# Optimization experiments

Hardware: AMD Instinct MI355X
Metric: run time of the kernel (lower is better)

Reference implementation:

```python
import jax, jax.numpy as jnp
import numpy as np
import math

N_HEAD = 4
NORM_GROUPS = 16
EPS = 1e-5


def setup_inputs() -> dict:
    key = jax.random.key(0)
    ks = jax.random.split(key, 4)
    B, C, H, W = 2, 256, 64, 64
    return {
        "input": jax.random.normal(ks[0], (B, C, H, W), dtype=jnp.float32),
        "gn_weight": jnp.ones((C,), dtype=jnp.float32),
        "gn_bias": jnp.zeros((C,), dtype=jnp.float32),
        # 1x1 convs are plain channel matmuls: weight [out_ch, in_ch]
        "qkv_weight": jax.random.normal(ks[1], (3 * C, C), dtype=jnp.float32) / math.sqrt(C),
        "out_weight": jax.random.normal(ks[2], (C, C), dtype=jnp.float32) / math.sqrt(C),
        "out_bias": jnp.zeros((C,), dtype=jnp.float32),
    }


def _group_norm(x, weight, bias):
    B, C, H, W = x.shape
    g = x.reshape(B, NORM_GROUPS, C // NORM_GROUPS, H, W)
    mu = g.mean(axis=(2, 3, 4), keepdims=True)
    var = g.var(axis=(2, 3, 4), keepdims=True)
    g = (g - mu) * jax.lax.rsqrt(var + EPS)
    return g.reshape(B, C, H, W) * weight[:, None, None] + bias[:, None, None]


def reference(input, gn_weight, gn_bias, qkv_weight, out_weight, out_bias):
    B, C, H, W = input.shape
    head_dim = C // N_HEAD
    x = _group_norm(input, gn_weight, gn_bias)
    # 1x1 conv (no bias) -> [B, 3C, H, W] -> [B, n_head, 3*head_dim, H, W]
    qkv = jnp.einsum('bchw,oc->bohw', x, qkv_weight)
    qkv = qkv.reshape(B, N_HEAD, 3 * head_dim, H, W)
    q, k, v = jnp.split(qkv, 3, axis=2)
    # full spatial attention; note: scale is sqrt(channel), as in the source
    attn = jnp.einsum('bnchw,bncyx->bnhwyx', q, k) / math.sqrt(C)
    attn = jax.nn.softmax(attn.reshape(B, N_HEAD, H, W, H * W), axis=-1)
    attn = attn.reshape(B, N_HEAD, H, W, H, W)
    out = jnp.einsum('bnhwyx,bncyx->bnchw', attn, v).reshape(B, C, H, W)
    out = jnp.einsum('bchw,oc->bohw', out, out_weight) + out_bias[:, None, None]
    return out + input
```

## Files before the change

### kernel.cpp

```cpp
#include <hip/hip_runtime.h>

typedef __bf16        bf16x8 __attribute__((ext_vector_type(8)));
typedef float         f32x4  __attribute__((ext_vector_type(4)));
typedef unsigned short u16x4 __attribute__((ext_vector_type(4)));
typedef unsigned short u16x8 __attribute__((ext_vector_type(8)));
typedef unsigned int  u32x4  __attribute__((ext_vector_type(4)));

#define MFMA16(a,b,c) __builtin_amdgcn_mfma_f32_16x16x32_bf16((a),(b),(c),0,0,0)

static __device__ __forceinline__ unsigned short f2bf(float f) {
  unsigned int u = __builtin_bit_cast(unsigned int, f);
  u += 0x7fffu + ((u >> 16) & 1u);
  return (unsigned short)(u >> 16);
}
static __device__ __forceinline__ unsigned int pk2rne(float a, float b) {
  return (unsigned int)f2bf(a) | ((unsigned int)f2bf(b) << 16);
}
static __device__ __forceinline__ unsigned int pkrn(float a, float b) {
#if __has_builtin(__builtin_amdgcn_cvt_pk_bf16_f32)
  auto r = __builtin_amdgcn_cvt_pk_bf16_f32(a, b);
  return __builtin_bit_cast(unsigned int, r);
#else
  return pk2rne(a, b);
#endif
}
static __device__ __forceinline__ bf16x8 as_bf(u32x4 v) {
  return __builtin_bit_cast(bf16x8, v);
}
static __device__ __forceinline__ float bf2f(unsigned short u) {
  return __builtin_bit_cast(float, ((unsigned int)u) << 16);
}

#define SDIM 4096
#define CDIM 256
#define NHEAD 4
#define HDIM 64
#define NBATCH 2
#define KSPLIT 4

__global__ __launch_bounds__(256) void k_prep(const float* __restrict__ x,
                                              const float* __restrict__ wq,
                                              const float* __restrict__ wo,
                                              unsigned short* __restrict__ wqf,
                                              unsigned short* __restrict__ wof,
                                              float2* __restrict__ Sp) {
  int j = blockIdx.x, i = threadIdx.x;
  if (j < 256) {
    const float* p = x + (size_t)(j >> 3) * 65536 + (size_t)(j & 7) * 8192;
    float s = 0.f, sq = 0.f;
#pragma unroll
    for (int r = 0; r < 8; ++r) {
      float4 v = *(const float4*)(p + (r * 256 + i) * 4);
      s  += v.x + v.y + v.z + v.w;
      sq += v.x * v.x + v.y * v.y + v.z * v.z + v.w * v.w;
    }
    __shared__ float rs[256], rq[256];
    rs[i] = s; rq[i] = sq;
    __syncthreads();
    for (int off = 128; off > 0; off >>= 1) {
      if (i < off) { rs[i] += rs[i + off]; rq[i] += rq[i + off]; }
      __syncthreads();
    }
    if (i == 0) Sp[j] = make_float2(rs[0], rq[0]);
  } else {
    int t = (j - 256) * 256 + i;
#pragma unroll
    for (int u = 0; u < 2; ++u) {
      int G = t * 2 + u;
      const float* src; unsigned short* dst;
      if (G < 24576) {
        int tile = G >> 6, l = G & 63;
        src = wq + (size_t)((tile >> 3) * 16 + (l & 15)) * 256 + (tile & 7) * 32 + (l >> 4) * 8;
        dst = wqf + (size_t)G * 8;
      } else {
        int G2 = G - 24576, tile = G2 >> 6, l = G2 & 63;
        src = wo + (size_t)((tile >> 3) * 16 + (l & 15)) * 256 + (tile & 7) * 32 + (l >> 4) * 8;
        dst = wof + (size_t)G2 * 8;
      }
      float4 v0 = *(const float4*)src, v1 = *(const float4*)(src + 4);
      u16x8 r;
      r[0] = f2bf(v0.x); r[1] = f2bf(v0.y); r[2] = f2bf(v0.z); r[3] = f2bf(v0.w);
      r[4] = f2bf(v1.x); r[5] = f2bf(v1.y); r[6] = f2bf(v1.z); r[7] = f2bf(v1.w);
      *(u16x8*)dst = r;
    }
  }
}

__global__ __launch_bounds__(256) void k_gn_apply(const float* __restrict__ x,
                                                  const float2* __restrict__ Sp,
                                                  const float* __restrict__ gnw,
                                                  const float* __restrict__ gnb,
                                                  unsigned short* __restrict__ Xf) {
  __shared__ __attribute__((aligned(16))) unsigned short sT[64 * 268];
  __shared__ float2 sStat[16];
  int b = blockIdx.y, s0 = blockIdx.x * 64;
  int i = threadIdx.x, lane = i & 63, w = i >> 6;
  if (i < 16) {
    float s = 0.f, sq = 0.f;
#pragma unroll
    for (int u = 0; u < 8; ++u) {
      float2 v = Sp[(b * 16 + i) * 8 + u];
      s += v.x; sq += v.y;
    }
    float mean = s * (1.f / 65536.f);
    float var  = sq * (1.f / 65536.f) - mean * mean;
    sStat[i] = make_float2(mean, rsqrtf(var + 1e-5f));
  }
  __syncthreads();
#pragma unroll 4
  for (int r = 0; r < 64; ++r) {
    int c = r * 4 + w;
    float v = x[((size_t)(b * CDIM + c)) * SDIM + s0 + lane];
    float2 st = sStat[c >> 4];
    float nv = (v - st.x) * st.y * gnw[c] + gnb[c];
    sT[lane * 268 + c] = f2bf(nv);
  }
  __syncthreads();
  int l = i & 63, fr = i >> 6;
#pragma unroll
  for (int g = 0; g < 8; ++g) {
    int tile = fr * 8 + g, st = tile >> 3, kc = tile & 7;
    const unsigned short* src = &sT[(st * 16 + (l & 15)) * 268 + kc * 32 + (l >> 4) * 8];
    u16x4 lo = *(const u16x4*)src, hi = *(const u16x4*)(src + 4);
    unsigned short* dst = Xf + (((size_t)(b * 256 + (s0 >> 4) + st) * 8 + kc) * 64 + l) * 8;
    *(u16x4*)dst = lo;
    *(u16x4*)(dst + 4) = hi;
  }
}

template <int M, int MODE>
__global__ __launch_bounds__(256) void k_gemm(const unsigned short* __restrict__ Wf,
                                              const unsigned short* __restrict__ Xf,
                                              unsigned short* __restrict__ Qf,
                                              unsigned short* __restrict__ Kf,
                                              unsigned short* __restrict__ Vf,
                                              float* __restrict__ outf,
                                              const float* __restrict__ bias,
                                              const float* __restrict__ resid) {
  __shared__ __attribute__((aligned(16))) unsigned short sB[64 * 68];
  int b = blockIdx.z, s0 = blockIdx.y * 64, o0 = blockIdx.x * 64;
  int i = threadIdx.x, lane = i & 63, w = i >> 6;
  int quad = lane >> 4, m = lane & 15;
  int ot = blockIdx.x * 4 + w;
  int stg = s0 >> 4;

  f32x4 acc[4] = {};
#pragma unroll
  for (int kc = 0; kc < 8; ++kc) {
    bf16x8 aW = as_bf(*(const u32x4*)(Wf + (((size_t)ot * 8 + kc) * 64 + lane) * 8));
#pragma unroll
    for (int st = 0; st < 4; ++st) {
      bf16x8 bX = as_bf(*(const u32x4*)(Xf + ((((size_t)b * 256 + stg + st) * 8 + kc) * 64 + lane) * 8));
      acc[st] = MFMA16(aW, bX, acc[st]);
    }
  }

  if (MODE == 1) {
#pragma unroll
    for (int st = 0; st < 4; ++st)
#pragma unroll
      for (int r = 0; r < 4; ++r) {
        int o = o0 + w * 16 + quad * 4 + r;
        int s = s0 + st * 16 + m;
        size_t idx = ((size_t)b * M + o) * SDIM + s;
        outf[idx] = acc[st][r] + bias[o] + resid[idx];
      }
  } else {
    int sec = (o0 >> 6) % 3;
    int h   = o0 / 192;
    int bh  = b * NHEAD + h;
    float qs = (sec == 0) ? 0.09016844f : 1.0f;
#pragma unroll
    for (int st = 0; st < 4; ++st) {
      uint2 pk = make_uint2(pk2rne(acc[st][0] * qs, acc[st][1] * qs),
                            pk2rne(acc[st][2] * qs, acc[st][3] * qs));
      *(uint2*)&sB[(st * 16 + m) * 68 + w * 16 + quad * 4] = pk;
    }
    __syncthreads();
    int lp = i & 63, qp = lp >> 4, mp = lp & 15, t = i >> 6;
    if (sec < 2) {
      unsigned short* base = (sec == 0) ? Qf : Kf;
#pragma unroll
      for (int ks = 0; ks < 2; ++ks) {
        const unsigned short* src = &sB[(t * 16 + mp) * 68 + ks * 32 + qp * 8];
        u16x4 lo = *(const u16x4*)src;
        u16x4 hi = *(const u16x4*)(src + 4);
        unsigned short* dst = base + ((((size_t)bh * 256 + (s0 >> 4) + t) * 2 + ks) * 64 + lp) * 8;
        *(u16x4*)dst = lo;
        *(u16x4*)(dst + 4) = hi;
      }
    } else {
      int kt32l = t >> 1, dts = (t & 1) * 2;
#pragma unroll
      for (int dd = 0; dd < 2; ++dd) {
        int dt = dts + dd;
        u16x8 v;
#pragma unroll
        for (int jj = 0; jj < 8; ++jj)
          v[jj] = sB[(kt32l * 32 + qp * 8 + jj) * 68 + dt * 16 + mp];
        unsigned short* dst = Vf + ((((size_t)bh * 128 + (s0 >> 5) + kt32l) * 4 + dt) * 64 + lp) * 8;
        *(u16x8*)dst = v;
      }
    }
  }
}

__global__ __launch_bounds__(256, 4) void k_attn(const unsigned short* __restrict__ Qf,
                                                 const unsigned short* __restrict__ Kf,
                                                 const unsigned short* __restrict__ Vf,
                                                 unsigned short* __restrict__ Opb,
                                                 float* __restrict__ Lp) {
  __shared__ __attribute__((aligned(16))) unsigned short sP[4][32 * 40];
  int bh = blockIdx.y, kk = blockIdx.z;
  int i = threadIdx.x, lane = i & 63, w = i >> 6;
  int quad = lane >> 4, m = lane & 15;
  constexpr int ITERS = SDIM / KSPLIT / 32;

  bf16x8 bq[2][2];
#pragma unroll
  for (int qt = 0; qt < 2; ++qt)
#pragma unroll
    for (int ks = 0; ks < 2; ++ks)
      bq[qt][ks] = as_bf(*(const u32x4*)(Qf +
        ((((size_t)bh * 256 + (blockIdx.x * 8 + w * 2 + qt)) * 2 + ks) * 64 + lane) * 8));

  bf16x8 aone;
  {
    u16x8 t;
#pragma unroll
    for (int jj = 0; jj < 8; ++jj) t[jj] = 0x3F80;
    aone = __builtin_bit_cast(bf16x8, t);
  }

  f32x4 oacc[2][4] = {};
  f32x4 liacc[2] = {};

  for (int it = 0; it < ITERS; ++it) {
    bf16x8 ak[2][2], av[4];
    int kb16 = kk * (ITERS * 2) + it * 2;
#pragma unroll
    for (int ky = 0; ky < 2; ++ky)
#pragma unroll
      for (int ks = 0; ks < 2; ++ks)
        ak[ky][ks] = as_bf(*(const u32x4*)(Kf +
          ((((size_t)bh * 256 + kb16 + ky) * 2 + ks) * 64 + lane) * 8));
    int kb32 = kk * ITERS + it;
#pragma unroll
    for (int dt = 0; dt < 4; ++dt)
      av[dt] = as_bf(*(const u32x4*)(Vf +
        ((((size_t)bh * 128 + kb32) * 4 + dt) * 64 + lane) * 8));

#pragma unroll
    for (int qt = 0; qt < 2; ++qt) {
      f32x4 sc0 = {-18.f, -18.f, -18.f, -18.f};
      f32x4 sc1 = sc0;
      sc0 = MFMA16(ak[0][0], bq[qt][0], sc0);
      sc0 = MFMA16(ak[0][1], bq[qt][1], sc0);
      sc1 = MFMA16(ak[1][0], bq[qt][0], sc1);
      sc1 = MFMA16(ak[1][1], bq[qt][1], sc1);
      float p[8];
#pragma unroll
      for (int r = 0; r < 4; ++r) {
        p[r]     = __builtin_amdgcn_exp2f(sc0[r]);
        p[4 + r] = __builtin_amdgcn_exp2f(sc1[r]);
      }
      int row = (qt * 16 + m) * 40;
      *(uint2*)&sP[w][row + quad * 4]      = make_uint2(pkrn(p[0], p[1]), pkrn(p[2], p[3]));
      *(uint2*)&sP[w][row + 16 + quad * 4] = make_uint2(pkrn(p[4], p[5]), pkrn(p[6], p[7]));
    }
#pragma unroll
    for (int qt = 0; qt < 2; ++qt) {
      bf16x8 bp = *(const bf16x8*)&sP[w][(qt * 16 + m) * 40 + quad * 8];
#pragma unroll
      for (int dt = 0; dt < 4; ++dt)
        oacc[qt][dt] = MFMA16(av[dt], bp, oacc[qt][dt]);
      liacc[qt] = MFMA16(aone, bp, liacc[qt]);
    }
  }

  size_t qg = (size_t)(kk * 8 + bh) * SDIM + blockIdx.x * 128 + w * 32;
  if (quad == 0) {
#pragma unroll
    for (int qt = 0; qt < 2; ++qt) Lp[qg + qt * 16 + m] = liacc[qt][0];
  }
#pragma unroll
  for (int qt = 0; qt < 2; ++qt)
#pragma unroll
    for (int dt = 0; dt < 4; ++dt) {
      uint2 pk = make_uint2(pk2rne(oacc[qt][dt][0], oacc[qt][dt][1]),
                            pk2rne(oacc[qt][dt][2], oacc[qt][dt][3]));
      *(uint2*)&Opb[(qg + qt * 16 + m) * 64 + dt * 16 + quad * 4] = pk;
    }
}

__global__ __launch_bounds__(256) void k_combine(const unsigned short* __restrict__ Opb,
                                                 const float* __restrict__ Lp,
                                                 unsigned short* __restrict__ aof) {
  int gid = blockIdx.x * 256 + threadIdx.x;
  int bh = gid >> 14, rem = gid & 16383, q = rem >> 2, dq = rem & 3;
  float li = 0.f, o[16];
#pragma unroll
  for (int e = 0; e < 16; ++e) o[e] = 0.f;
#pragma unroll
  for (int ks = 0; ks < KSPLIT; ++ks) {
    size_t base = (size_t)(ks * 8 + bh) * SDIM + q;
    li += Lp[base];
    const unsigned short* p = Opb + base * 64 + dq * 16;
    u16x8 a = *(const u16x8*)p, b2 = *(const u16x8*)(p + 8);
#pragma unroll
    for (int e = 0; e < 8; ++e) { o[e] += bf2f(a[e]); o[8 + e] += bf2f(b2[e]); }
  }
  float inv = 1.f / li;
  unsigned int dw[8];
#pragma unroll
  for (int e = 0; e < 8; ++e) dw[e] = pk2rne(o[2 * e] * inv, o[2 * e + 1] * inv);
  int b = bh >> 2, c0 = (bh & 3) * 64 + dq * 16;
  int st = q >> 4, mm = q & 15, kc = c0 >> 5, qd = (c0 >> 3) & 3;
  unsigned short* base = aof + (((size_t)(b * 256 + st) * 8 + kc) * 64) * 8;
  *(u32x4*)(base + (qd * 16 + mm) * 8)       = u32x4{dw[0], dw[1], dw[2], dw[3]};
  *(u32x4*)(base + ((qd + 1) * 16 + mm) * 8) = u32x4{dw[4], dw[5], dw[6], dw[7]};
}

extern "C" void kernel_launch(void* const* d_in, const int* in_sizes, int n_in,
                              void* d_out, int out_size, void* d_ws, size_t ws_size,
                              hipStream_t stream) {
  const float* input = (const float*)d_in[0];
  const float* gnw   = (const float*)d_in[1];
  const float* gnb   = (const float*)d_in[2];
  const float* wq    = (const float*)d_in[3];
  const float* wo    = (const float*)d_in[4];
  const float* ob    = (const float*)d_in[5];
  float* out = (float*)d_out;

  char* ws = (char*)d_ws;
  unsigned short* Xf  = (unsigned short*)(ws);
  unsigned short* Qf  = (unsigned short*)(ws + (4ull  << 20));
  unsigned short* Kf  = (unsigned short*)(ws + (8ull  << 20));
  unsigned short* Vf  = (unsigned short*)(ws + (12ull << 20));
  unsigned short* aof = (unsigned short*)(ws + (16ull << 20));
  unsigned short* wqf = (unsigned short*)(ws + (20ull << 20));
  unsigned short* wof = (unsigned short*)(ws + (20ull << 20) + (1u << 19));
  float2* Sp          = (float2*)(ws + (20ull << 20) + (3u << 18));
  float* Lp           = (float*)(ws + (21ull << 20));
  unsigned short* Opb = (unsigned short*)(ws + (22ull << 20));

  k_prep<<<320, 256, 0, stream>>>(input, wq, wo, wqf, wof, Sp);
  k_gn_apply<<<dim3(64, NBATCH), 256, 0, stream>>>(input, Sp, gnw, gnb, Xf);
  k_gemm<768, 0><<<dim3(12, 64, NBATCH), 256, 0, stream>>>(wqf, Xf, Qf, Kf, Vf, nullptr, nullptr, nullptr);
  k_attn<<<dim3(32, NHEAD * NBATCH, KSPLIT), 256, 0, stream>>>(Qf, Kf, Vf, Opb, Lp);
  k_combine<<<512, 256, 0, stream>>>(Opb, Lp, aof);
  k_gemm<256, 1><<<dim3(4, 64, NBATCH), 256, 0, stream>>>(wof, aof, nullptr, nullptr, nullptr, out, ob, input);
}
```

Measured before the change: 148.5 us.

## Fuse split-K combine into output projection and software-pipeline K loads in attention

Removes the separate combine kernel. The output projection GEMM now reads the per-split partial attention outputs directly, accumulates one result per head, and applies each head's 1/l normalisation before adding bias and residual. In the attention kernel, the MFMA that computed the softmax denominator from a ones matrix is replaced by a scalar sum plus cross-lane shuffles. K-tile loads are double-buffered so they run one iteration ahead. The projection does KSPLIT times more MFMAs and loads, and holds 16 accumulators per wave, which raises register pressure.

```diff
diff --git a/kernel.cpp b/kernel.cpp
--- a/kernel.cpp
+++ b/kernel.cpp
@@ -128,15 +128,11 @@
   }
 }
 
-template <int M, int MODE>
-__global__ __launch_bounds__(256) void k_gemm(const unsigned short* __restrict__ Wf,
-                                              const unsigned short* __restrict__ Xf,
-                                              unsigned short* __restrict__ Qf,
-                                              unsigned short* __restrict__ Kf,
-                                              unsigned short* __restrict__ Vf,
-                                              float* __restrict__ outf,
-                                              const float* __restrict__ bias,
-                                              const float* __restrict__ resid) {
+__global__ __launch_bounds__(256) void k_qkv(const unsigned short* __restrict__ Wf,
+                                             const unsigned short* __restrict__ Xf,
+                                             unsigned short* __restrict__ Qf,
+                                             unsigned short* __restrict__ Kf,
+                                             unsigned short* __restrict__ Vf) {
   __shared__ __attribute__((aligned(16))) unsigned short sB[64 * 68];
   int b = blockIdx.z, s0 = blockIdx.y * 64, o0 = blockIdx.x * 64;
   int i = threadIdx.x, lane = i & 63, w = i >> 6;
@@ -155,52 +151,40 @@
     }
   }
 
-  if (MODE == 1) {
-#pragma unroll
-    for (int st = 0; st < 4; ++st)
-#pragma unroll
-      for (int r = 0; r < 4; ++r) {
-        int o = o0 + w * 16 + quad * 4 + r;
-        int s = s0 + st * 16 + m;
-        size_t idx = ((size_t)b * M + o) * SDIM + s;
-        outf[idx] = acc[st][r] + bias[o] + resid[idx];
-      }
+  int sec = (o0 >> 6) % 3;
+  int h   = o0 / 192;
+  int bh  = b * NHEAD + h;
+  float qs = (sec == 0) ? 0.09016844f : 1.0f;
+#pragma unroll
+  for (int st = 0; st < 4; ++st) {
+    uint2 pk = make_uint2(pk2rne(acc[st][0] * qs, acc[st][1] * qs),
+                          pk2rne(acc[st][2] * qs, acc[st][3] * qs));
+    *(uint2*)&sB[(st * 16 + m) * 68 + w * 16 + quad * 4] = pk;
+  }
+  __syncthreads();
+  int lp = i & 63, qp = lp >> 4, mp = lp & 15, t = i >> 6;
+  if (sec < 2) {
+    unsigned short* base = (sec == 0) ? Qf : Kf;
+#pragma unroll
+    for (int ks = 0; ks < 2; ++ks) {
+      const unsigned short* src = &sB[(t * 16 + mp) * 68 + ks * 32 + qp * 8];
+      u16x4 lo = *(const u16x4*)src;
+      u16x4 hi = *(const u16x4*)(src + 4);
+      unsigned short* dst = base + ((((size_t)bh * 256 + (s0 >> 4) + t) * 2 + ks) * 64 + lp) * 8;
+      *(u16x4*)dst = lo;
+      *(u16x4*)(dst + 4) = hi;
+    }
   } else {
-    int sec = (o0 >> 6) % 3;
-    int h   = o0 / 192;
-    int bh  = b * NHEAD + h;
-    float qs = (sec == 0) ? 0.09016844f : 1.0f;
-#pragma unroll
-    for (int st = 0; st < 4; ++st) {
-      uint2 pk = make_uint2(pk2rne(acc[st][0] * qs, acc[st][1] * qs),
-                            pk2rne(acc[st][2] * qs, acc[st][3] * qs));
-      *(uint2*)&sB[(st * 16 + m) * 68 + w * 16 + quad * 4] = pk;
-    }
-    __syncthreads();
-    int lp = i & 63, qp = lp >> 4, mp = lp & 15, t = i >> 6;
-    if (sec < 2) {
-      unsigned short* base = (sec == 0) ? Qf : Kf;
-#pragma unroll
-      for (int ks = 0; ks < 2; ++ks) {
-        const unsigned short* src = &sB[(t * 16 + mp) * 68 + ks * 32 + qp * 8];
-        u16x4 lo = *(const u16x4*)src;
-        u16x4 hi = *(const u16x4*)(src + 4);
-        unsigned short* dst = base + ((((size_t)bh * 256 + (s0 >> 4) + t) * 2 + ks) * 64 + lp) * 8;
-        *(u16x4*)dst = lo;
-        *(u16x4*)(dst + 4) = hi;
-      }
-    } else {
-      int kt32l = t >> 1, dts = (t & 1) * 2;
-#pragma unroll
-      for (int dd = 0; dd < 2; ++dd) {
-        int dt = dts + dd;
-        u16x8 v;
-#pragma unroll
-        for (int jj = 0; jj < 8; ++jj)
-          v[jj] = sB[(kt32l * 32 + qp * 8 + jj) * 68 + dt * 16 + mp];
-        unsigned short* dst = Vf + ((((size_t)bh * 128 + (s0 >> 5) + kt32l) * 4 + dt) * 64 + lp) * 8;
-        *(u16x8*)dst = v;
-      }
+    int kt32l = t >> 1, dts = (t & 1) * 2;
+#pragma unroll
+    for (int dd = 0; dd < 2; ++dd) {
+      int dt = dts + dd;
+      u16x8 v;
+#pragma unroll
+      for (int jj = 0; jj < 8; ++jj)
+        v[jj] = sB[(kt32l * 32 + qp * 8 + jj) * 68 + dt * 16 + mp];
+      unsigned short* dst = Vf + ((((size_t)bh * 128 + (s0 >> 5) + kt32l) * 4 + dt) * 64 + lp) * 8;
+      *(u16x8*)dst = v;
     }
   }
 }
@@ -224,26 +208,23 @@
       bq[qt][ks] = as_bf(*(const u32x4*)(Qf +
         ((((size_t)bh * 256 + (blockIdx.x * 8 + w * 2 + qt)) * 2 + ks) * 64 + lane) * 8));
 
-  bf16x8 aone;
-  {
-    u16x8 t;
-#pragma unroll
-    for (int jj = 0; jj < 8; ++jj) t[jj] = 0x3F80;
-    aone = __builtin_bit_cast(bf16x8, t);
-  }
-
   f32x4 oacc[2][4] = {};
-  f32x4 liacc[2] = {};
-
-  for (int it = 0; it < ITERS; ++it) {
-    bf16x8 ak[2][2], av[4];
+  float li[2] = {0.f, 0.f};
+
+  bf16x8 akb[2][2][2];
+
+  auto loadK = [&](int it, int par) {
     int kb16 = kk * (ITERS * 2) + it * 2;
 #pragma unroll
     for (int ky = 0; ky < 2; ++ky)
 #pragma unroll
       for (int ks = 0; ks < 2; ++ks)
-        ak[ky][ks] = as_bf(*(const u32x4*)(Kf +
+        akb[par][ky][ks] = as_bf(*(const u32x4*)(Kf +
           ((((size_t)bh * 256 + kb16 + ky) * 2 + ks) * 64 + lane) * 8));
+  };
+
+  auto body = [&](int it, int par) {
+    bf16x8 av[4];
     int kb32 = kk * ITERS + it;
 #pragma unroll
     for (int dt = 0; dt < 4; ++dt)
@@ -254,16 +235,17 @@
     for (int qt = 0; qt < 2; ++qt) {
       f32x4 sc0 = {-18.f, -18.f, -18.f, -18.f};
       f32x4 sc1 = sc0;
-      sc0 = MFMA16(ak[0][0], bq[qt][0], sc0);
-      sc0 = MFMA16(ak[0][1], bq[qt][1], sc0);
-      sc1 = MFMA16(ak[1][0], bq[qt][0], sc1);
-      sc1 = MFMA16(ak[1][1], bq[qt][1], sc1);
+      sc0 = MFMA16(akb[par][0][0], bq[qt][0], sc0);
+      sc0 = MFMA16(akb[par][0][1], bq[qt][1], sc0);
+      sc1 = MFMA16(akb[par][1][0], bq[qt][0], sc1);
+      sc1 = MFMA16(akb[par][1][1], bq[qt][1], sc1);
       float p[8];
 #pragma unroll
       for (int r = 0; r < 4; ++r) {
         p[r]     = __builtin_amdgcn_exp2f(sc0[r]);
         p[4 + r] = __builtin_amdgcn_exp2f(sc1[r]);
       }
+      li[qt] += ((p[0] + p[1]) + (p[2] + p[3])) + ((p[4] + p[5]) + (p[6] + p[7]));
       int row = (qt * 16 + m) * 40;
       *(uint2*)&sP[w][row + quad * 4]      = make_uint2(pkrn(p[0], p[1]), pkrn(p[2], p[3]));
       *(uint2*)&sP[w][row + 16 + quad * 4] = make_uint2(pkrn(p[4], p[5]), pkrn(p[6], p[7]));
@@ -274,14 +256,26 @@
 #pragma unroll
       for (int dt = 0; dt < 4; ++dt)
         oacc[qt][dt] = MFMA16(av[dt], bp, oacc[qt][dt]);
-      liacc[qt] = MFMA16(aone, bp, liacc[qt]);
-    }
+    }
+  };
+
+  loadK(0, 0);
+  for (int it = 0; it < ITERS; it += 2) {
+    loadK(it + 1, 1);
+    body(it, 0);
+    if (it + 2 < ITERS) loadK(it + 2, 0);
+    body(it + 1, 1);
   }
 
   size_t qg = (size_t)(kk * 8 + bh) * SDIM + blockIdx.x * 128 + w * 32;
+#pragma unroll
+  for (int qt = 0; qt < 2; ++qt) {
+    li[qt] += __shfl_xor(li[qt], 16);
+    li[qt] += __shfl_xor(li[qt], 32);
+  }
   if (quad == 0) {
 #pragma unroll
-    for (int qt = 0; qt < 2; ++qt) Lp[qg + qt * 16 + m] = liacc[qt][0];
+    for (int qt = 0; qt < 2; ++qt) Lp[qg + qt * 16 + m] = li[qt];
   }
 #pragma unroll
   for (int qt = 0; qt < 2; ++qt)
@@ -293,32 +287,56 @@
     }
 }
 
-__global__ __launch_bounds__(256) void k_combine(const unsigned short* __restrict__ Opb,
-                                                 const float* __restrict__ Lp,
-                                                 unsigned short* __restrict__ aof) {
-  int gid = blockIdx.x * 256 + threadIdx.x;
-  int bh = gid >> 14, rem = gid & 16383, q = rem >> 2, dq = rem & 3;
-  float li = 0.f, o[16];
-#pragma unroll
-  for (int e = 0; e < 16; ++e) o[e] = 0.f;
-#pragma unroll
-  for (int ks = 0; ks < KSPLIT; ++ks) {
-    size_t base = (size_t)(ks * 8 + bh) * SDIM + q;
-    li += Lp[base];
-    const unsigned short* p = Opb + base * 64 + dq * 16;
-    u16x8 a = *(const u16x8*)p, b2 = *(const u16x8*)(p + 8);
-#pragma unroll
-    for (int e = 0; e < 8; ++e) { o[e] += bf2f(a[e]); o[8 + e] += bf2f(b2[e]); }
-  }
-  float inv = 1.f / li;
-  unsigned int dw[8];
-#pragma unroll
-  for (int e = 0; e < 8; ++e) dw[e] = pk2rne(o[2 * e] * inv, o[2 * e + 1] * inv);
-  int b = bh >> 2, c0 = (bh & 3) * 64 + dq * 16;
-  int st = q >> 4, mm = q & 15, kc = c0 >> 5, qd = (c0 >> 3) & 3;
-  unsigned short* base = aof + (((size_t)(b * 256 + st) * 8 + kc) * 64) * 8;
-  *(u32x4*)(base + (qd * 16 + mm) * 8)       = u32x4{dw[0], dw[1], dw[2], dw[3]};
-  *(u32x4*)(base + ((qd + 1) * 16 + mm) * 8) = u32x4{dw[4], dw[5], dw[6], dw[7]};
+__global__ __launch_bounds__(256) void k_proj(const unsigned short* __restrict__ Wf,
+                                              const unsigned short* __restrict__ Opb,
+                                              const float* __restrict__ Lp,
+                                              const float* __restrict__ bias,
+                                              const float* __restrict__ resid,
+                                              float* __restrict__ out) {
+  int b = blockIdx.z, s0 = blockIdx.y * 64, o0 = blockIdx.x * 64;
+  int i = threadIdx.x, lane = i & 63, w = i >> 6;
+  int quad = lane >> 4, m = lane & 15;
+  int ot = blockIdx.x * 4 + w;
+
+  f32x4 acc[4][4] = {};
+#pragma unroll
+  for (int kc = 0; kc < 8; ++kc) {
+    bf16x8 aW = as_bf(*(const u32x4*)(Wf + (((size_t)ot * 8 + kc) * 64 + lane) * 8));
+    int h = kc >> 1;
+#pragma unroll
+    for (int kkq = 0; kkq < KSPLIT; ++kkq) {
+#pragma unroll
+      for (int st = 0; st < 4; ++st) {
+        const unsigned short* p = Opb +
+          ((size_t)(kkq * 8 + b * NHEAD + h) * SDIM + s0 + st * 16 + m) * 64 +
+          (kc & 1) * 32 + quad * 8;
+        bf16x8 bX = as_bf(*(const u32x4*)p);
+        acc[h][st] = MFMA16(aW, bX, acc[h][st]);
+      }
+    }
+  }
+
+  float inv[4][4];
+#pragma unroll
+  for (int h = 0; h < 4; ++h)
+#pragma unroll
+    for (int st = 0; st < 4; ++st) {
+      size_t base = (size_t)(b * NHEAD + h) * SDIM + s0 + st * 16 + m;
+      float l = Lp[base] + Lp[base + 8ull * SDIM] + Lp[base + 16ull * SDIM] + Lp[base + 24ull * SDIM];
+      inv[h][st] = 1.f / l;
+    }
+
+#pragma unroll
+  for (int st = 0; st < 4; ++st)
+#pragma unroll
+    for (int r = 0; r < 4; ++r) {
+      int o = o0 + w * 16 + quad * 4 + r;
+      int s = s0 + st * 16 + m;
+      float v = acc[0][st][r] * inv[0][st] + acc[1][st][r] * inv[1][st] +
+                acc[2][st][r] * inv[2][st] + acc[3][st][r] * inv[3][st];
+      size_t idx = ((size_t)b * CDIM + o) * SDIM + s;
+      out[idx] = v + bias[o] + resid[idx];
+    }
 }
 
 extern "C" void kernel_launch(void* const* d_in, const int* in_sizes, int n_in,
@@ -337,7 +355,6 @@
   unsigned short* Qf  = (unsigned short*)(ws + (4ull  << 20));
   unsigned short* Kf  = (unsigned short*)(ws + (8ull  << 20));
   unsigned short* Vf  = (unsigned short*)(ws + (12ull << 20));
-  unsigned short* aof = (unsigned short*)(ws + (16ull << 20));
   unsigned short* wqf = (unsigned short*)(ws + (20ull << 20));
   unsigned short* wof = (unsigned short*)(ws + (20ull << 20) + (1u << 19));
   float2* Sp          = (float2*)(ws + (20ull << 20) + (3u << 18));
@@ -346,8 +363,7 @@
 
   k_prep<<<320, 256, 0, stream>>>(input, wq, wo, wqf, wof, Sp);
   k_gn_apply<<<dim3(64, NBATCH), 256, 0, stream>>>(input, Sp, gnw, gnb, Xf);
-  k_gemm<768, 0><<<dim3(12, 64, NBATCH), 256, 0, stream>>>(wqf, Xf, Qf, Kf, Vf, nullptr, nullptr, nullptr);
+  k_qkv<<<dim3(12, 64, NBATCH), 256, 0, stream>>>(wqf, Xf, Qf, Kf, Vf);
   k_attn<<<dim3(32, NHEAD * NBATCH, KSPLIT), 256, 0, stream>>>(Qf, Kf, Vf, Opb, Lp);
-  k_combine<<<512, 256, 0, stream>>>(Opb, Lp, aof);
-  k_gemm<256, 1><<<dim3(4, 64, NBATCH), 256, 0, stream>>>(wof, aof, nullptr, nullptr, nullptr, out, ob, input);
-}
+  k_proj<<<dim3(4, 64, NBATCH), 256, 0, stream>>>(wof, Opb, Lp, ob, input, out);
+}
```

Measured after the change: 223.4 us. 50.5% more time.
